# Kernel optimization log

Measured on AMD Instinct MI355X. Metric: run time of the kernel, lower is better.

The kernel has to match this reference:

```python
import jax, jax.numpy as jnp
import numpy as np

HIDDEN = 1024
N_HEADS = 16
HEAD_DIM = HIDDEN // N_HEADS  # 64
B, N = 2, 2048
SCALE = HIDDEN ** (-0.5)  # NOTE: original scales by full hidden_size, not head_dim


def setup_inputs() -> dict:
    key = jax.random.key(0)
    k1, k2 = jax.random.split(key)
    hidden_states = jax.random.normal(k1, (B, N, HIDDEN), dtype=jnp.float32)
    attention_mask = jnp.ones((B, N), dtype=jnp.int32)
    # per-head no-bias Linear(hidden -> 3*head_dim), stacked: [h, hidden, 3*head_dim]
    W_qkv = jax.random.normal(k2, (N_HEADS, HIDDEN, 3 * HEAD_DIM), dtype=jnp.float32) * (HIDDEN ** -0.5)
    return {"hidden_states": hidden_states, "attention_mask": attention_mask, "W_qkv": W_qkv}


def reference(hidden_states, attention_mask, W_qkv):
    # qkv: [b, h, n, 3*d]
    qkv = jnp.einsum('bnD,hDe->bhne', hidden_states, W_qkv)
    q, k, v = jnp.split(qkv, 3, axis=-1)  # each [b, h, n, d]
    scores = jnp.einsum('bhid,bhjd->bhij', q, k) * SCALE
    mask = attention_mask[:, None, None, :] == 0  # [b,1,1,n]
    scores = jnp.where(mask, -jnp.inf, scores)
    attn = jax.nn.softmax(scores, axis=-1)
    out = jnp.einsum('bhij,bhjd->bhid', attn, v)  # [b, h, n, d]
    # rearrange 'b h n d -> b n (h d)'
    return jnp.transpose(out, (0, 2, 1, 3)).reshape(out.shape[0], out.shape[2], -1)
```

## Files before the change

### kernel.cpp

```cpp
#include <hip/hip_runtime.h>
#include <hip/hip_bf16.h>


#define NH   16
#define HD   64
#define SEQ  2048
#define HID  1024
#define E3   192
#define QSCALE 0.04508422017f
#define MBIAS  -43.2808512f

typedef __attribute__((ext_vector_type(8)))  short short8;
typedef __attribute__((ext_vector_type(4)))  float f32x4;
typedef __attribute__((ext_vector_type(16))) float f32x16;
typedef unsigned short ushort_t;

#define MFMA16(a, b, c) __builtin_amdgcn_mfma_f32_16x16x32_bf16((a), (b), (c), 0, 0, 0)
#define MFMA32(a, b, c) __builtin_amdgcn_mfma_f32_32x32x16_bf16((a), (b), (c), 0, 0, 0)

#if __has_builtin(__builtin_amdgcn_exp2f)
#define EXP2(x) __builtin_amdgcn_exp2f(x)
#else
#define EXP2(x) exp2f(x)
#endif

static __device__ __forceinline__ ushort_t f2bf(float x) {
    unsigned u = __builtin_bit_cast(unsigned, x);
    unsigned r = u + 0x7fff + ((u >> 16) & 1);
    return (ushort_t)(r >> 16);
}

static __device__ __forceinline__ unsigned pack_trunc(float hi, float lo) {
#if __has_builtin(__builtin_amdgcn_perm)
    return __builtin_amdgcn_perm(__builtin_bit_cast(unsigned, hi),
                                 __builtin_bit_cast(unsigned, lo), 0x07060302u);
#else
    return (__builtin_bit_cast(unsigned, hi) & 0xffff0000u) |
           (__builtin_bit_cast(unsigned, lo) >> 16);
#endif
}

static __device__ __forceinline__ void load_lds16(const void* g, void* l) {
    __builtin_amdgcn_global_load_lds(
        (__attribute__((address_space(1))) void*)(g),
        (__attribute__((address_space(3))) void*)(l), 16, 0, 0);
}

__global__ __launch_bounds__(256) void k_cvt_x(const void* __restrict__ Xv,
                                               ushort_t* __restrict__ Xb,
                                               int* __restrict__ flagp) {
    __shared__ int cnt;
    if (threadIdx.x == 0) cnt = 0;
    __syncthreads();
    const unsigned* X32 = (const unsigned*)Xv;
    if (threadIdx.x < 64) {
        unsigned u = X32[(size_t)blockIdx.x * 2048 + threadIdx.x * 32 + 7];
        int bexp = (u >> 7) & 0xFF;
        if (bexp >= 0x68 && bexp <= 0x90) atomicAdd(&cnt, 1);
    }
    __syncthreads();
    const int isf32 = (cnt < 32);
    if (blockIdx.x == 0 && threadIdx.x == 0) *flagp = isf32;

    const size_t base = ((size_t)blockIdx.x * 256 + threadIdx.x) * 16;
    if (isf32) {
        const float* Xf = (const float*)Xv;
        ushort_t tmp[16];
#pragma unroll
        for (int c = 0; c < 4; ++c) {
            float4 v = *(const float4*)(Xf + base + c * 4);
            tmp[c * 4 + 0] = f2bf(v.x); tmp[c * 4 + 1] = f2bf(v.y);
            tmp[c * 4 + 2] = f2bf(v.z); tmp[c * 4 + 3] = f2bf(v.w);
        }
        *(float4*)(Xb + base)     = ((const float4*)tmp)[0];
        *(float4*)(Xb + base + 8) = ((const float4*)tmp)[1];
    } else {
        const ushort_t* Xh = (const ushort_t*)Xv;
        *(float4*)(Xb + base)     = *(const float4*)(Xh + base);
        *(float4*)(Xb + base + 8) = *(const float4*)(Xh + base + 8);
    }
}

__global__ __launch_bounds__(256) void k_cvt_w(const void* __restrict__ Wv,
                                               ushort_t* __restrict__ Wt,
                                               const int* __restrict__ flagp) {
    __shared__ ushort_t tile[64][72];
    const int isf32 = *flagp;
    const int h  = blockIdx.x;
    const int dt = blockIdx.y;
    const int et = blockIdx.z;
    const int D0 = dt * 64, e0 = et * 64;
    const int t  = threadIdx.x;
#pragma unroll
    for (int r = 0; r < 2; ++r) {
        int row = r * 32 + (t >> 3);
        int col = (t & 7) * 8;
        size_t base = ((size_t)(h * HID + D0 + row)) * E3 + e0 + col;
        if (isf32) {
            const float* Wf = (const float*)Wv;
            float4 a = *(const float4*)(Wf + base);
            float4 c = *(const float4*)(Wf + base + 4);
            tile[row][col + 0] = f2bf(a.x); tile[row][col + 1] = f2bf(a.y);
            tile[row][col + 2] = f2bf(a.z); tile[row][col + 3] = f2bf(a.w);
            tile[row][col + 4] = f2bf(c.x); tile[row][col + 5] = f2bf(c.y);
            tile[row][col + 6] = f2bf(c.z); tile[row][col + 7] = f2bf(c.w);
        } else {
            *(float4*)&tile[row][col] = *(const float4*)((const ushort_t*)Wv + base);
        }
    }
    __syncthreads();
#pragma unroll
    for (int r = 0; r < 2; ++r) {
        int erow = r * 32 + (t >> 3);
        int dcol = (t & 7) * 8;
        ushort_t vals[8];
#pragma unroll
        for (int i = 0; i < 8; ++i) vals[i] = tile[dcol + i][erow];
        *(float4*)(Wt + ((size_t)(h * E3 + e0 + erow)) * HID + D0 + dcol) = *(float4*)vals;
    }
}

__global__ __launch_bounds__(256) void k_qkv(const ushort_t* __restrict__ Xb,
                                             const ushort_t* __restrict__ Wt,
                                             ushort_t* __restrict__ Qb,
                                             ushort_t* __restrict__ Kb,
                                             ushort_t* __restrict__ Vtb) {
    __shared__ __align__(16) ushort_t smem[2 * 128 * 64];
    ushort_t* Xl = smem;
    ushort_t* Wl = smem + 128 * 64;

    const int e0 = blockIdx.x * 128;
    const int m0 = blockIdx.y * 128;
    const int b  = m0 >> 11;
    const int n0 = m0 & 2047;
    const int t = threadIdx.x;
    const int w = t >> 6, lane = t & 63, l15 = lane & 15, quad = lane >> 4;
    const int wrow0 = (w & 1) * 64, wcol0 = (w >> 1) * 64;
    const int srow = lane >> 3;
    const int scb  = (lane & 7) ^ srow;

    f32x4 acc[4][4];
#pragma unroll
    for (int i = 0; i < 4; ++i)
#pragma unroll
        for (int j = 0; j < 4; ++j) acc[i][j] = (f32x4){0.f, 0.f, 0.f, 0.f};

    for (int k0 = 0; k0 < HID; k0 += 64) {
        __syncthreads();
#pragma unroll
        for (int cc = 0; cc < 4; ++cc) {
            const int ch  = w * 4 + cc;
            const int row = ch * 8 + srow;
            load_lds16(Xb + (size_t)(m0 + row) * HID + k0 + scb * 8, &Xl[ch * 512]);
            load_lds16(Wt + (size_t)(e0 + row) * HID + k0 + scb * 8, &Wl[ch * 512]);
        }
        __syncthreads();
#pragma unroll
        for (int kh = 0; kh < 2; ++kh) {
            short8 af[4], bfm[4];
#pragma unroll
            for (int i = 0; i < 4; ++i) {
                const int r = wrow0 + i * 16 + l15;
                af[i] = *(const short8*)&Xl[r * 64 + ((kh * 4 + quad) ^ (r & 7)) * 8];
            }
#pragma unroll
            for (int j = 0; j < 4; ++j) {
                const int r = wcol0 + j * 16 + l15;
                bfm[j] = *(const short8*)&Wl[r * 64 + ((kh * 4 + quad) ^ (r & 7)) * 8];
            }
#pragma unroll
            for (int i = 0; i < 4; ++i)
#pragma unroll
                for (int j = 0; j < 4; ++j)
                    acc[i][j] = MFMA16(af[i], bfm[j], acc[i][j]);
        }
    }

    ushort_t* Vbuf = smem;
    __syncthreads();
#pragma unroll
    for (int i = 0; i < 4; ++i) {
#pragma unroll
        for (int j = 0; j < 4; ++j) {
            const int E0v = e0 + wcol0 + j * 16;
            const int hh  = E0v / 192;
            const int r0  = E0v - hh * 192;
            const int bh  = b * NH + hh;
            const int nb  = n0 + wrow0 + i * 16 + quad * 4;
            if (r0 < 64) {
                const int e = r0 + l15;
#pragma unroll
                for (int reg = 0; reg < 4; ++reg)
                    Qb[((size_t)bh * SEQ + nb + reg) * HD + e] = f2bf(acc[i][j][reg] * QSCALE);
            } else if (r0 < 128) {
                const int e = r0 - 64 + l15;
#pragma unroll
                for (int reg = 0; reg < 4; ++reg)
                    Kb[((size_t)bh * SEQ + nb + reg) * HD + e] = f2bf(acc[i][j][reg]);
            } else {
                const int d  = r0 - 128 + l15;
                const int nl = wrow0 + i * 16 + quad * 4;
#pragma unroll
                for (int reg = 0; reg < 4; ++reg)
                    Vbuf[d * 136 + nl + reg] = f2bf(acc[i][j][reg]);
            }
        }
    }
    const int m3 = blockIdx.x % 3;
    if (m3 != 0) {
        __syncthreads();
        const int hv  = (e0 + ((m3 == 1) ? 0 : 64)) / 192;
        const int bhv = b * NH + hv;
        const int dr = t >> 2, part = t & 3;
        size_t dst = ((size_t)bhv * HD + dr) * SEQ + n0 + part * 32;
#pragma unroll
        for (int c = 0; c < 4; ++c) {
            float4 v = *(const float4*)&Vbuf[dr * 136 + part * 32 + c * 8];
            *(float4*)(Vtb + dst + c * 8) = v;
        }
    }
}

__global__ __launch_bounds__(256) void k_attn(const ushort_t* __restrict__ Qb,
                                              const ushort_t* __restrict__ Kb,
                                              const ushort_t* __restrict__ Vtb,
                                              const int* __restrict__ mask,
                                              void* __restrict__ outv,
                                              const int* __restrict__ flagp) {
    __shared__ __align__(16) char smem_raw[75776];
    ushort_t* Pl    = (ushort_t*)(smem_raw + 49152);
    float*    biasl = (float*)(smem_raw + 67584);

    const int isf32 = *flagp;
    const int q0 = blockIdx.x * 128;
    const int bh = blockIdx.y;
    const int b  = bh >> 4, h = bh & 15;
    const int t  = threadIdx.x;
    const int w  = t >> 6, lane = t & 63;
    const int l31 = lane & 31, half = lane >> 5;
    const int srow = lane >> 3;
    const int scb  = (lane & 7) ^ srow;
    const int prow = w * 32 + l31;

    const f32x16 zero16 = {0.f,0.f,0.f,0.f,0.f,0.f,0.f,0.f,
                           0.f,0.f,0.f,0.f,0.f,0.f,0.f,0.f};

#pragma unroll
    for (int tj = 0; tj < 2; ++tj) {
        ushort_t* kb = (ushort_t*)(smem_raw + tj * 16384);
        ushort_t* vb = kb + 4096;
#pragma unroll
        for (int c = 0; c < 2; ++c) {
            const int ch  = w * 2 + c;
            const int row = ch * 8 + srow;
            load_lds16(Kb  + ((size_t)bh * SEQ + tj * 64 + row) * HD + scb * 8, &kb[ch * 512]);
            load_lds16(Vtb + ((size_t)bh * HD + row) * SEQ + tj * 64 + scb * 8, &vb[ch * 512]);
        }
    }

    int lm = 0;
    for (int i = t; i < SEQ; i += 256) {
        int mv = mask[b * SEQ + i];
        biasl[i] = mv ? 0.0f : MBIAS;
        lm |= (mv == 0);
    }
    short8 qa[4];
#pragma unroll
    for (int s = 0; s < 4; ++s)
        qa[s] = *(const short8*)(Qb + ((size_t)bh * SEQ + q0 + prow) * HD + s * 16 + half * 8);

    const int use_bias = __syncthreads_or(lm);

    f32x16 o[2];
    o[0] = zero16; o[1] = zero16;
    float l_r = 0.f;

    for (int j0 = 0; j0 < SEQ; j0 += 64) {
        const int idx = (j0 >> 6) % 3;
        if (j0 + 64 < SEQ) { asm volatile("s_waitcnt vmcnt(4)" ::: "memory"); }
        else               { asm volatile("s_waitcnt vmcnt(0)" ::: "memory"); }
        __builtin_amdgcn_s_barrier();
        asm volatile("" ::: "memory");
        if (j0 + 128 < SEQ) {
            ushort_t* kb = (ushort_t*)(smem_raw + ((idx + 2) % 3) * 16384);
            ushort_t* vb = kb + 4096;
#pragma unroll
            for (int c = 0; c < 2; ++c) {
                const int ch  = w * 2 + c;
                const int row = ch * 8 + srow;
                load_lds16(Kb  + ((size_t)bh * SEQ + j0 + 128 + row) * HD + scb * 8, &kb[ch * 512]);
                load_lds16(Vtb + ((size_t)bh * HD + row) * SEQ + j0 + 128 + scb * 8, &vb[ch * 512]);
            }
        }
        ushort_t* kb = (ushort_t*)(smem_raw + idx * 16384);
        ushort_t* vb = kb + 4096;

        f32x16 st[2];
#pragma unroll
        for (int kt = 0; kt < 2; ++kt) {
            const int rk = kt * 32 + l31;
            st[kt] = zero16;
#pragma unroll
            for (int s = 0; s < 4; ++s) {
                short8 ka = *(const short8*)&kb[rk * 64 + ((2 * s + half) ^ (rk & 7)) * 8];
                st[kt] = MFMA32(ka, qa[s], st[kt]);
            }
        }
        if (use_bias) {
#pragma unroll
            for (int kt = 0; kt < 2; ++kt)
#pragma unroll
                for (int g = 0; g < 4; ++g) {
                    float4 bj = *(const float4*)&biasl[j0 + kt * 32 + g * 8 + 4 * half];
#pragma unroll
                    for (int i = 0; i < 4; ++i)
                        st[kt][g * 4 + i] += ((const float*)&bj)[i];
                }
        }

#pragma unroll
        for (int kt = 0; kt < 2; ++kt) {
            float p[16];
#pragma unroll
            for (int r = 0; r < 16; ++r) { p[r] = EXP2(st[kt][r]); l_r += p[r]; }
#pragma unroll
            for (int g = 0; g < 4; ++g) {
                uint2 u;
                u.x = pack_trunc(p[4 * g + 1], p[4 * g + 0]);
                u.y = pack_trunc(p[4 * g + 3], p[4 * g + 2]);
                *(uint2*)&Pl[prow * 72 + kt * 32 + g * 8 + 4 * half] = u;
            }
        }
        short8 pb[4];
#pragma unroll
        for (int s = 0; s < 4; ++s)
            pb[s] = *(const short8*)&Pl[prow * 72 + s * 16 + half * 8];

#pragma unroll
        for (int dt = 0; dt < 2; ++dt) {
            const int rv = dt * 32 + l31;
#pragma unroll
            for (int s = 0; s < 4; ++s) {
                short8 va = *(const short8*)&vb[rv * 64 + ((2 * s + half) ^ (rv & 7)) * 8];
                o[dt] = MFMA32(va, pb[s], o[dt]);
            }
        }
    }

    l_r += __shfl_xor(l_r, 32);
    const float rinv = 1.0f / l_r;

    __syncthreads();
    const int r = t >> 1, part = t & 1;
    if (!isf32) {
        ushort_t* Ol = (ushort_t*)smem_raw;
#pragma unroll
        for (int dt = 0; dt < 2; ++dt)
#pragma unroll
            for (int g = 0; g < 4; ++g) {
                uint2 u;
                u.x = (unsigned)f2bf(o[dt][4 * g + 0] * rinv) |
                      ((unsigned)f2bf(o[dt][4 * g + 1] * rinv) << 16);
                u.y = (unsigned)f2bf(o[dt][4 * g + 2] * rinv) |
                      ((unsigned)f2bf(o[dt][4 * g + 3] * rinv) << 16);
                *(uint2*)&Ol[prow * 72 + dt * 32 + g * 8 + 4 * half] = u;
            }
        __syncthreads();
        ushort_t* outp = (ushort_t*)outv;
        size_t dst = ((size_t)b * SEQ + q0 + r) * HID + h * HD + part * 32;
#pragma unroll
        for (int c = 0; c < 4; ++c) {
            float4 v = *(const float4*)&Ol[r * 72 + part * 32 + c * 8];
            *(float4*)(outp + dst + c * 8) = v;
        }
    } else {
        float* Olf = (float*)smem_raw;
#pragma unroll
        for (int dt = 0; dt < 2; ++dt)
#pragma unroll
            for (int g = 0; g < 4; ++g) {
                float2 v0 = {o[dt][4 * g + 0] * rinv, o[dt][4 * g + 1] * rinv};
                float2 v1 = {o[dt][4 * g + 2] * rinv, o[dt][4 * g + 3] * rinv};
                *(float2*)&Olf[prow * 68 + dt * 32 + g * 8 + 4 * half]     = v0;
                *(float2*)&Olf[prow * 68 + dt * 32 + g * 8 + 4 * half + 2] = v1;
            }
        __syncthreads();
        float* outp = (float*)outv;
        size_t dst = ((size_t)b * SEQ + q0 + r) * HID + h * HD + part * 32;
#pragma unroll
        for (int c = 0; c < 8; ++c) {
            float4 v = *(const float4*)&Olf[r * 68 + part * 32 + c * 4];
            *(float4*)(outp + dst + c * 4) = v;
        }
    }
}

extern "C" void kernel_launch(void* const* d_in, const int* in_sizes, int n_in,
                              void* d_out, int out_size, void* d_ws, size_t ws_size,
                              hipStream_t stream) {
    const void* X    = d_in[0];
    const int*  mask = (const int*)d_in[1];
    const void* W    = d_in[2];

    char* ws = (char*)d_ws;
    ushort_t* Qb    = (ushort_t*)(ws);
    ushort_t* Kb    = (ushort_t*)(ws + 8388608);
    ushort_t* Vtb   = (ushort_t*)(ws + 16777216);
    ushort_t* Wtb   = (ushort_t*)(ws + 25165824);
    int*      flagp = (int*)(ws + 31457280);
    ushort_t* Xb    = (ushort_t*)d_out;

    k_cvt_x<<<1024, 256, 0, stream>>>(X, Xb, flagp);
    k_cvt_w<<<dim3(16, 16, 3), 256, 0, stream>>>(W, Wtb, flagp);
    k_qkv<<<dim3(24, 32), 256, 0, stream>>>(Xb, Wtb, Qb, Kb, Vtb);
    k_attn<<<dim3(16, 32), 256, 0, stream>>>(Qb, Kb, Vtb, mask, d_out, flagp);
}
```

Before: 184.3 us.

## Split KV range across two wave groups in attention block and merge partials

The attention kernel now launches 512 threads per block, arranged as two groups of four waves. Each group processes half of the key sequence with 32-key tiles and its own triple-buffered LDS ring. After the loop, the second group writes its unnormalized output and row sums to LDS, and the first group combines them, normalizes and stages the result for the store. The goal is more waves in flight per block to hide latency and keep the MFMA units busy. In exchange there are smaller tiles with more barriers per key processed, an extra merge step, and more register and LDS pressure.

```diff
diff --git a/kernel.cpp b/kernel.cpp
--- a/kernel.cpp
+++ b/kernel.cpp
@@ -221,15 +221,14 @@
     }
 }
 
-__global__ __launch_bounds__(256) void k_attn(const ushort_t* __restrict__ Qb,
+__global__ __launch_bounds__(512) void k_attn(const ushort_t* __restrict__ Qb,
                                               const ushort_t* __restrict__ Kb,
                                               const ushort_t* __restrict__ Vtb,
                                               const int* __restrict__ mask,
                                               void* __restrict__ outv,
                                               const int* __restrict__ flagp) {
-    __shared__ __align__(16) char smem_raw[75776];
-    ushort_t* Pl    = (ushort_t*)(smem_raw + 49152);
-    float*    biasl = (float*)(smem_raw + 67584);
+    __shared__ __align__(16) char smem_raw[77824];
+    float* biasl = (float*)(smem_raw + 69632);
 
     const int isf32 = *flagp;
     const int q0 = blockIdx.x * 128;
@@ -238,28 +237,29 @@
     const int t  = threadIdx.x;
     const int w  = t >> 6, lane = t & 63;
     const int l31 = lane & 31, half = lane >> 5;
-    const int srow = lane >> 3;
-    const int scb  = (lane & 7) ^ srow;
-    const int prow = w * 32 + l31;
+    const int g   = w >> 2, wg = w & 3;
+    const int prow = wg * 32 + l31;
+    const int kbase = g * 1024;
+    char* bufs = smem_raw + g * 24576;
+    ushort_t* Pl = (ushort_t*)(smem_raw + 49152 + g * 10240);
+
+    const int ksr = lane >> 3, kcb = (lane & 7) ^ ksr;
+    const int vdr = lane >> 2, vcb = (lane & 3) ^ (vdr & 3);
 
     const f32x16 zero16 = {0.f,0.f,0.f,0.f,0.f,0.f,0.f,0.f,
                            0.f,0.f,0.f,0.f,0.f,0.f,0.f,0.f};
 
 #pragma unroll
     for (int tj = 0; tj < 2; ++tj) {
-        ushort_t* kb = (ushort_t*)(smem_raw + tj * 16384);
-        ushort_t* vb = kb + 4096;
-#pragma unroll
-        for (int c = 0; c < 2; ++c) {
-            const int ch  = w * 2 + c;
-            const int row = ch * 8 + srow;
-            load_lds16(Kb  + ((size_t)bh * SEQ + tj * 64 + row) * HD + scb * 8, &kb[ch * 512]);
-            load_lds16(Vtb + ((size_t)bh * HD + row) * SEQ + tj * 64 + scb * 8, &vb[ch * 512]);
-        }
+        ushort_t* kb = (ushort_t*)(bufs + tj * 8192);
+        ushort_t* vb = kb + 2048;
+        const int j0g = kbase + tj * 32;
+        load_lds16(Kb  + ((size_t)bh * SEQ + j0g + wg * 8 + ksr) * HD + kcb * 8, &kb[wg * 512]);
+        load_lds16(Vtb + ((size_t)bh * HD + wg * 16 + vdr) * SEQ + j0g + vcb * 8, &vb[wg * 512]);
     }
 
     int lm = 0;
-    for (int i = t; i < SEQ; i += 256) {
+    for (int i = t; i < SEQ; i += 512) {
         int mv = mask[b * SEQ + i];
         biasl[i] = mv ? 0.0f : MBIAS;
         lm |= (mv == 0);
@@ -275,121 +275,131 @@
     o[0] = zero16; o[1] = zero16;
     float l_r = 0.f;
 
-    for (int j0 = 0; j0 < SEQ; j0 += 64) {
-        const int idx = (j0 >> 6) % 3;
-        if (j0 + 64 < SEQ) { asm volatile("s_waitcnt vmcnt(4)" ::: "memory"); }
-        else               { asm volatile("s_waitcnt vmcnt(0)" ::: "memory"); }
+    for (int it = 0; it < 32; ++it) {
+        const int idx = it % 3;
+        if (it < 31) { asm volatile("s_waitcnt vmcnt(2)" ::: "memory"); }
+        else         { asm volatile("s_waitcnt vmcnt(0)" ::: "memory"); }
         __builtin_amdgcn_s_barrier();
         asm volatile("" ::: "memory");
-        if (j0 + 128 < SEQ) {
-            ushort_t* kb = (ushort_t*)(smem_raw + ((idx + 2) % 3) * 16384);
-            ushort_t* vb = kb + 4096;
-#pragma unroll
-            for (int c = 0; c < 2; ++c) {
-                const int ch  = w * 2 + c;
-                const int row = ch * 8 + srow;
-                load_lds16(Kb  + ((size_t)bh * SEQ + j0 + 128 + row) * HD + scb * 8, &kb[ch * 512]);
-                load_lds16(Vtb + ((size_t)bh * HD + row) * SEQ + j0 + 128 + scb * 8, &vb[ch * 512]);
-            }
-        }
-        ushort_t* kb = (ushort_t*)(smem_raw + idx * 16384);
-        ushort_t* vb = kb + 4096;
-
-        f32x16 st[2];
-#pragma unroll
-        for (int kt = 0; kt < 2; ++kt) {
-            const int rk = kt * 32 + l31;
-            st[kt] = zero16;
-#pragma unroll
-            for (int s = 0; s < 4; ++s) {
-                short8 ka = *(const short8*)&kb[rk * 64 + ((2 * s + half) ^ (rk & 7)) * 8];
-                st[kt] = MFMA32(ka, qa[s], st[kt]);
-            }
+        if (it < 30) {
+            ushort_t* kb = (ushort_t*)(bufs + ((idx + 2) % 3) * 8192);
+            ushort_t* vb = kb + 2048;
+            const int j0g = kbase + (it + 2) * 32;
+            load_lds16(Kb  + ((size_t)bh * SEQ + j0g + wg * 8 + ksr) * HD + kcb * 8, &kb[wg * 512]);
+            load_lds16(Vtb + ((size_t)bh * HD + wg * 16 + vdr) * SEQ + j0g + vcb * 8, &vb[wg * 512]);
+        }
+        ushort_t* kb = (ushort_t*)(bufs + idx * 8192);
+        ushort_t* vb = kb + 2048;
+        const int j0g = kbase + it * 32;
+
+        f32x16 st = zero16;
+#pragma unroll
+        for (int s = 0; s < 4; ++s) {
+            short8 ka = *(const short8*)&kb[l31 * 64 + ((2 * s + half) ^ (l31 & 7)) * 8];
+            st = MFMA32(ka, qa[s], st);
         }
         if (use_bias) {
 #pragma unroll
-            for (int kt = 0; kt < 2; ++kt)
-#pragma unroll
-                for (int g = 0; g < 4; ++g) {
-                    float4 bj = *(const float4*)&biasl[j0 + kt * 32 + g * 8 + 4 * half];
-#pragma unroll
-                    for (int i = 0; i < 4; ++i)
-                        st[kt][g * 4 + i] += ((const float*)&bj)[i];
-                }
-        }
-
-#pragma unroll
-        for (int kt = 0; kt < 2; ++kt) {
-            float p[16];
-#pragma unroll
-            for (int r = 0; r < 16; ++r) { p[r] = EXP2(st[kt][r]); l_r += p[r]; }
-#pragma unroll
-            for (int g = 0; g < 4; ++g) {
-                uint2 u;
-                u.x = pack_trunc(p[4 * g + 1], p[4 * g + 0]);
-                u.y = pack_trunc(p[4 * g + 3], p[4 * g + 2]);
-                *(uint2*)&Pl[prow * 72 + kt * 32 + g * 8 + 4 * half] = u;
-            }
-        }
-        short8 pb[4];
-#pragma unroll
-        for (int s = 0; s < 4; ++s)
-            pb[s] = *(const short8*)&Pl[prow * 72 + s * 16 + half * 8];
+            for (int g4 = 0; g4 < 4; ++g4) {
+                float4 bj = *(const float4*)&biasl[j0g + g4 * 8 + 4 * half];
+#pragma unroll
+                for (int i = 0; i < 4; ++i)
+                    st[g4 * 4 + i] += ((const float*)&bj)[i];
+            }
+        }
+
+        float p[16];
+#pragma unroll
+        for (int r = 0; r < 16; ++r) { p[r] = EXP2(st[r]); l_r += p[r]; }
+#pragma unroll
+        for (int g4 = 0; g4 < 4; ++g4) {
+            uint2 u;
+            u.x = pack_trunc(p[4 * g4 + 1], p[4 * g4 + 0]);
+            u.y = pack_trunc(p[4 * g4 + 3], p[4 * g4 + 2]);
+            *(uint2*)&Pl[prow * 40 + g4 * 8 + 4 * half] = u;
+        }
+        short8 pb[2];
+#pragma unroll
+        for (int s = 0; s < 2; ++s)
+            pb[s] = *(const short8*)&Pl[prow * 40 + s * 16 + half * 8];
 
 #pragma unroll
         for (int dt = 0; dt < 2; ++dt) {
             const int rv = dt * 32 + l31;
 #pragma unroll
-            for (int s = 0; s < 4; ++s) {
-                short8 va = *(const short8*)&vb[rv * 64 + ((2 * s + half) ^ (rv & 7)) * 8];
+            for (int s = 0; s < 2; ++s) {
+                short8 va = *(const short8*)&vb[rv * 32 + ((2 * s + half) ^ (rv & 3)) * 8];
                 o[dt] = MFMA32(va, pb[s], o[dt]);
             }
         }
     }
 
     l_r += __shfl_xor(l_r, 32);
-    const float rinv = 1.0f / l_r;
-
-    __syncthreads();
-    const int r = t >> 1, part = t & 1;
+
+    float* Obuf = (float*)smem_raw;
+    float* lbuf = (float*)(smem_raw + 73728);
+    __syncthreads();
+    if (g == 1) {
+#pragma unroll
+        for (int dt = 0; dt < 2; ++dt)
+#pragma unroll
+            for (int g4 = 0; g4 < 4; ++g4) {
+                float4 v = {o[dt][4 * g4 + 0], o[dt][4 * g4 + 1],
+                            o[dt][4 * g4 + 2], o[dt][4 * g4 + 3]};
+                *(float4*)&Obuf[prow * 68 + dt * 32 + g4 * 8 + 4 * half] = v;
+            }
+        if (half == 0) lbuf[prow] = l_r;
+    }
+    __syncthreads();
+    if (g == 0) {
+        const float rinv = 1.0f / (l_r + lbuf[prow]);
+        if (!isf32) {
+            ushort_t* Ol = (ushort_t*)(smem_raw + 36864);
+#pragma unroll
+            for (int dt = 0; dt < 2; ++dt)
+#pragma unroll
+                for (int g4 = 0; g4 < 4; ++g4) {
+                    float4 v = *(const float4*)&Obuf[prow * 68 + dt * 32 + g4 * 8 + 4 * half];
+                    uint2 u;
+                    u.x = (unsigned)f2bf((o[dt][4 * g4 + 0] + v.x) * rinv) |
+                          ((unsigned)f2bf((o[dt][4 * g4 + 1] + v.y) * rinv) << 16);
+                    u.y = (unsigned)f2bf((o[dt][4 * g4 + 2] + v.z) * rinv) |
+                          ((unsigned)f2bf((o[dt][4 * g4 + 3] + v.w) * rinv) << 16);
+                    *(uint2*)&Ol[prow * 72 + dt * 32 + g4 * 8 + 4 * half] = u;
+                }
+        } else {
+            float* Olf = (float*)(smem_raw + 36864);
+#pragma unroll
+            for (int dt = 0; dt < 2; ++dt)
+#pragma unroll
+                for (int g4 = 0; g4 < 4; ++g4) {
+                    float4 v = *(const float4*)&Obuf[prow * 68 + dt * 32 + g4 * 8 + 4 * half];
+                    float4 r;
+                    r.x = (o[dt][4 * g4 + 0] + v.x) * rinv;
+                    r.y = (o[dt][4 * g4 + 1] + v.y) * rinv;
+                    r.z = (o[dt][4 * g4 + 2] + v.z) * rinv;
+                    r.w = (o[dt][4 * g4 + 3] + v.w) * rinv;
+                    *(float4*)&Olf[prow * 68 + dt * 32 + g4 * 8 + 4 * half] = r;
+                }
+        }
+    }
+    __syncthreads();
+    const int r = t >> 2, part = t & 3;
     if (!isf32) {
-        ushort_t* Ol = (ushort_t*)smem_raw;
-#pragma unroll
-        for (int dt = 0; dt < 2; ++dt)
-#pragma unroll
-            for (int g = 0; g < 4; ++g) {
-                uint2 u;
-                u.x = (unsigned)f2bf(o[dt][4 * g + 0] * rinv) |
-                      ((unsigned)f2bf(o[dt][4 * g + 1] * rinv) << 16);
-                u.y = (unsigned)f2bf(o[dt][4 * g + 2] * rinv) |
-                      ((unsigned)f2bf(o[dt][4 * g + 3] * rinv) << 16);
-                *(uint2*)&Ol[prow * 72 + dt * 32 + g * 8 + 4 * half] = u;
-            }
-        __syncthreads();
+        ushort_t* Ol = (ushort_t*)(smem_raw + 36864);
         ushort_t* outp = (ushort_t*)outv;
-        size_t dst = ((size_t)b * SEQ + q0 + r) * HID + h * HD + part * 32;
+        size_t dst = ((size_t)b * SEQ + q0 + r) * HID + h * HD + part * 16;
+        float4 v0 = *(const float4*)&Ol[r * 72 + part * 16];
+        float4 v1 = *(const float4*)&Ol[r * 72 + part * 16 + 8];
+        *(float4*)(outp + dst)     = v0;
+        *(float4*)(outp + dst + 8) = v1;
+    } else {
+        float* Olf = (float*)(smem_raw + 36864);
+        float* outp = (float*)outv;
+        size_t dst = ((size_t)b * SEQ + q0 + r) * HID + h * HD + part * 16;
 #pragma unroll
         for (int c = 0; c < 4; ++c) {
-            float4 v = *(const float4*)&Ol[r * 72 + part * 32 + c * 8];
-            *(float4*)(outp + dst + c * 8) = v;
-        }
-    } else {
-        float* Olf = (float*)smem_raw;
-#pragma unroll
-        for (int dt = 0; dt < 2; ++dt)
-#pragma unroll
-            for (int g = 0; g < 4; ++g) {
-                float2 v0 = {o[dt][4 * g + 0] * rinv, o[dt][4 * g + 1] * rinv};
-                float2 v1 = {o[dt][4 * g + 2] * rinv, o[dt][4 * g + 3] * rinv};
-                *(float2*)&Olf[prow * 68 + dt * 32 + g * 8 + 4 * half]     = v0;
-                *(float2*)&Olf[prow * 68 + dt * 32 + g * 8 + 4 * half + 2] = v1;
-            }
-        __syncthreads();
-        float* outp = (float*)outv;
-        size_t dst = ((size_t)b * SEQ + q0 + r) * HID + h * HD + part * 32;
-#pragma unroll
-        for (int c = 0; c < 8; ++c) {
-            float4 v = *(const float4*)&Olf[r * 68 + part * 32 + c * 4];
+            float4 v = *(const float4*)&Olf[r * 68 + part * 16 + c * 4];
             *(float4*)(outp + dst + c * 4) = v;
         }
     }
@@ -413,5 +423,5 @@
     k_cvt_x<<<1024, 256, 0, stream>>>(X, Xb, flagp);
     k_cvt_w<<<dim3(16, 16, 3), 256, 0, stream>>>(W, Wtb, flagp);
     k_qkv<<<dim3(24, 32), 256, 0, stream>>>(Xb, Wtb, Qb, Kb, Vtb);
-    k_attn<<<dim3(16, 32), 256, 0, stream>>>(Qb, Kb, Vtb, mask, d_out, flagp);
-}
+    k_attn<<<dim3(16, 32), 512, 0, stream>>>(Qb, Kb, Vtb, mask, d_out, flagp);
+}
```

Measured after the change: 180.8 us. No clear change (-1.9%).
